# Kernel tuning notes

Hardware: AMD Instinct MI355X
Metric: run time of the kernel (lower is better)

The kernel has to match this reference:

```python
import jax, jax.numpy as jnp
import numpy as np

HIDDEN = 1024
NH = 16
NKV = 8
HD = 128
ROPE_BASE = 1e6
EPS = 1e-6


def _rms_norm(x, w):
    # x: [..., HD], norm in fp32 like the torch module
    xf = x.astype(jnp.float32)
    var = jnp.mean(xf * xf, axis=-1, keepdims=True)
    return w * (xf * jax.lax.rsqrt(var + EPS)).astype(x.dtype)


def _rotate_half(x):
    h = x.shape[-1] // 2
    return jnp.concatenate([-x[..., h:], x[..., :h]], axis=-1)


def _rope_cos_sin(position_ids, dtype):
    inv_freq = 1.0 / (ROPE_BASE ** (jnp.arange(0, HD, 2, dtype=jnp.float32) / HD))
    freqs = position_ids.astype(jnp.float32)[:, None] * inv_freq[None, :]  # [S, HD/2]
    emb = jnp.concatenate([freqs, freqs], axis=-1)  # [S, HD]
    return jnp.cos(emb).astype(dtype), jnp.sin(emb).astype(dtype)


def setup_inputs() -> dict:
    key = jax.random.key(0)
    ks = jax.random.split(key, 7)
    B, S = 2, 2048
    scale = lambda fan_in: 1.0 / np.sqrt(fan_in)
    return {
        "hidden_states": jax.random.normal(ks[0], (B, S, HIDDEN), jnp.float32),
        "position_ids": jnp.arange(S, dtype=jnp.int32),
        "Wq": jax.random.normal(ks[1], (HIDDEN, NH * HD), jnp.float32) * scale(HIDDEN),
        "Wk": jax.random.normal(ks[2], (HIDDEN, NKV * HD), jnp.float32) * scale(HIDDEN),
        "Wv": jax.random.normal(ks[3], (HIDDEN, NKV * HD), jnp.float32) * scale(HIDDEN),
        "Wo": jax.random.normal(ks[4], (NH * HD, HIDDEN), jnp.float32) * scale(NH * HD),
        "q_norm_w": jnp.ones((HD,), jnp.float32),
        "k_norm_w": jnp.ones((HD,), jnp.float32),
    }


def reference(hidden_states, position_ids, Wq, Wk, Wv, Wo, q_norm_w, k_norm_w):
    B, S, _ = hidden_states.shape
    G = NH // NKV  # GQA group size

    q = (hidden_states @ Wq).reshape(B, S, NH, HD)
    k = (hidden_states @ Wk).reshape(B, S, NKV, HD)
    v = (hidden_states @ Wv).reshape(B, S, NKV, HD)

    q = _rms_norm(q, q_norm_w).transpose(0, 2, 1, 3)  # [B, NH, S, HD]
    k = _rms_norm(k, k_norm_w).transpose(0, 2, 1, 3)  # [B, NKV, S, HD]
    v = v.transpose(0, 2, 1, 3)                        # [B, NKV, S, HD]

    cos, sin = _rope_cos_sin(position_ids, q.dtype)    # [S, HD] each
    q = q * cos + _rotate_half(q) * sin
    k = k * cos + _rotate_half(k) * sin

    # GQA: broadcast KV heads across groups instead of repeat_interleave copies
    qg = q.reshape(B, NKV, G, S, HD)
    scores = jnp.einsum('bkgsd,bknd->bkgsn', qg, k) / jnp.sqrt(jnp.float32(HD))
    causal = jnp.tril(jnp.ones((S, S), dtype=bool))
    scores = jnp.where(causal, scores, -jnp.inf)
    attn = jax.nn.softmax(scores, axis=-1)
    out = jnp.einsum('bkgsn,bknd->bkgsd', attn, v)  # [B, NKV, G, S, HD]
    out = out.reshape(B, NH, S, HD).transpose(0, 2, 1, 3).reshape(B, S, NH * HD)
    return out @ Wo
```

## Files before the change

### kernel.cpp

```cpp
#include <hip/hip_runtime.h>
#include <cstdint>
#include <cstddef>

#define HIDDEN 1024
#define NH 16
#define NKV 8
#define HD 128
#define SEQ 2048
#define BATCH 2
#define NTOK (BATCH*SEQ)

typedef __bf16 bf16x8 __attribute__((ext_vector_type(8)));
typedef float f32x4 __attribute__((ext_vector_type(4)));

__device__ __forceinline__ unsigned short f2bf(float f) {
  unsigned int u = __float_as_uint(f);
  u += 0x7FFFu + ((u >> 16) & 1u);
  return (unsigned short)(u >> 16);
}
__device__ __forceinline__ float bf2f(unsigned short h) {
  return __uint_as_float(((unsigned int)h) << 16);
}

#if __has_builtin(__builtin_amdgcn_exp2f)
#define EXP2(x) __builtin_amdgcn_exp2f(x)
#else
#define EXP2(x) exp2f(x)
#endif

__device__ __forceinline__ void glds16(const unsigned short* g, unsigned short* l) {
  __builtin_amdgcn_global_load_lds(
      (const __attribute__((address_space(1))) unsigned int*)g,
      (__attribute__((address_space(3))) unsigned int*)l, 16, 0, 0);
}

#define WAIT_VM8()   __builtin_amdgcn_s_waitcnt(0x0F78)
#define WAIT_VM4()   __builtin_amdgcn_s_waitcnt(0x0F74)
#define WAIT_VM0()   __builtin_amdgcn_s_waitcnt(0x0F70)
#define WAIT_LGKM0() __builtin_amdgcn_s_waitcnt(0xC07F)
#define BARRIER()    __builtin_amdgcn_s_barrier()

__device__ __forceinline__ float dpp_addx1(float x) {
  int v = __builtin_amdgcn_update_dpp(0, __float_as_int(x), 0xB1, 0xF, 0xF, true);
  return x + __int_as_float(v);
}

__global__ __launch_bounds__(256) void tcvt_all_kernel(
    const float* __restrict__ Wq, const float* __restrict__ Wk,
    const float* __restrict__ Wv, const float* __restrict__ Wo,
    const float* __restrict__ hs,
    unsigned short* __restrict__ wqkvt, unsigned short* __restrict__ wot,
    unsigned short* __restrict__ hsb) {
  const int i = blockIdx.x;
  const int tx = threadIdx.x, ty = threadIdx.y;
  if (i >= 6144) {
    const int t = ty*32 + tx;
    const size_t base = (size_t)(i - 6144) * 1024;
#pragma unroll
    for (int j = 0; j < 4; ++j) {
      const size_t idx = base + j*256 + t;
      float4 v = ((const float4*)hs)[idx];
      ushort4 o;
      o.x = f2bf(v.x); o.y = f2bf(v.y); o.z = f2bf(v.z); o.w = f2bf(v.w);
      ((ushort4*)hsb)[idx] = o;
    }
    return;
  }
  __shared__ float tl[32][33];
  const float* src; unsigned short* dst; int R, C, r0, c0;
  if (i < 2048)      { int l = i;        src = Wq; dst = wqkvt;                      R = 1024; C = 2048; r0 = (l & 31)*32; c0 = (l >> 5)*32; }
  else if (i < 3072) { int l = i - 2048; src = Wk; dst = wqkvt + (size_t)2048*1024;  R = 1024; C = 1024; r0 = (l & 31)*32; c0 = (l >> 5)*32; }
  else if (i < 4096) { int l = i - 3072; src = Wv; dst = wqkvt + (size_t)3072*1024;  R = 1024; C = 1024; r0 = (l & 31)*32; c0 = (l >> 5)*32; }
  else               { int l = i - 4096; src = Wo; dst = wot;                        R = 2048; C = 1024; r0 = (l & 63)*32; c0 = (l >> 6)*32; }
#pragma unroll
  for (int k = 0; k < 4; ++k)
    tl[ty + 8*k][tx] = src[(size_t)(r0 + ty + 8*k)*C + c0 + tx];
  __syncthreads();
#pragma unroll
  for (int k = 0; k < 4; ++k)
    dst[(size_t)(c0 + ty + 8*k)*R + r0 + tx] = f2bf(tl[tx][ty + 8*k]);
}

__global__ __launch_bounds__(256) void gemm_qkv_fused_kernel(
    const unsigned short* __restrict__ A,
    const unsigned short* __restrict__ Bt,
    const float* __restrict__ qw, const float* __restrict__ kw,
    const int* __restrict__ pos_ids,
    unsigned short* __restrict__ q_l,
    unsigned short* __restrict__ k_l,
    unsigned short* __restrict__ vt8) {
  constexpr int BM = 128, BK = 64, K = 1024, NIT = K/BK;
  constexpr int FS = 132;
  __shared__ __align__(16) char smem[70144];
  unsigned short* As0 = (unsigned short*)smem;
  unsigned short* Bs0 = (unsigned short*)(smem + 32768);
  float* ftile = (float*)smem;
  float* rinv  = (float*)(smem + 69632);

  const int t = threadIdx.x, lane = t & 63, w = t >> 6;
  const int l15 = lane & 15, l4 = lane >> 4;
  const int wr = (w >> 1)*64, wc = (w & 1)*64;
  const int m0 = blockIdx.x * BM, n0 = blockIdx.y * 128;
  const unsigned short* Ab = A + (size_t)m0*K;
  const unsigned short* Bb = Bt + (size_t)n0*K;

  const f32x4 vzero = {0.f, 0.f, 0.f, 0.f};
  f32x4 acc[4][4];
#pragma unroll
  for (int i = 0; i < 4; ++i)
#pragma unroll
    for (int j = 0; j < 4; ++j) acc[i][j] = vzero;

#pragma unroll
  for (int i = 0; i < 4; ++i) {
    const int c = (w*4 + i)*64 + lane;
    glds16(Ab + (size_t)(c >> 3)*K + ((c ^ (c >> 3)) & 7)*8, As0 + (size_t)(w*4 + i)*512);
  }
#pragma unroll
  for (int i = 0; i < 4; ++i) {
    const int c = (w*4 + i)*64 + lane;
    glds16(Bb + (size_t)(c >> 3)*K + ((c ^ (c >> 3)) & 7)*8, Bs0 + (size_t)(w*4 + i)*512);
  }

  for (int kb = 0; kb < NIT; ++kb) {
    const int cur = kb & 1;
    WAIT_LGKM0(); BARRIER();
    if (kb + 1 < NIT) {
      const int kn = (kb + 1) * BK;
      const int nb = (cur^1)*8192;
#pragma unroll
      for (int i = 0; i < 4; ++i) {
        const int c = (w*4 + i)*64 + lane;
        glds16(Ab + (size_t)(c >> 3)*K + kn + ((c ^ (c >> 3)) & 7)*8, As0 + nb + (size_t)(w*4 + i)*512);
      }
#pragma unroll
      for (int i = 0; i < 4; ++i) {
        const int c = (w*4 + i)*64 + lane;
        glds16(Bb + (size_t)(c >> 3)*K + kn + ((c ^ (c >> 3)) & 7)*8, Bs0 + nb + (size_t)(w*4 + i)*512);
      }
      WAIT_VM8();
    } else {
      WAIT_VM0();
    }
    BARRIER();

    const unsigned short* Ac = As0 + cur*8192;
    const unsigned short* Bc = Bs0 + cur*8192;
#pragma unroll
    for (int kk = 0; kk < 2; ++kk) {
      const int kc = kk*4 + l4;
      bf16x8 af[4], bfr[4];
#pragma unroll
      for (int i = 0; i < 4; ++i) {
        int m = wr + i*16 + l15;
        af[i] = *(const bf16x8*)(Ac + ((size_t)m*8 + (kc ^ (m & 7)))*8);
      }
#pragma unroll
      for (int j = 0; j < 4; ++j) {
        int n = wc + j*16 + l15;
        bfr[j] = *(const bf16x8*)(Bc + ((size_t)n*8 + (kc ^ (n & 7)))*8);
      }
#pragma unroll
      for (int i = 0; i < 4; ++i)
#pragma unroll
        for (int j = 0; j < 4; ++j)
          acc[i][j] = __builtin_amdgcn_mfma_f32_16x16x32_bf16(af[i], bfr[j], acc[i][j], 0, 0, 0);
    }
  }

  WAIT_LGKM0(); BARRIER();
#pragma unroll
  for (int i = 0; i < 4; ++i)
#pragma unroll
    for (int j = 0; j < 4; ++j)
#pragma unroll
      for (int r = 0; r < 4; ++r) {
        const int row = wr + i*16 + l4*4 + r;
        const int col = wc + j*16 + l15;
        ftile[row*FS + col] = acc[i][j][r];
      }
  WAIT_LGKM0(); BARRIER();

  const int ny = n0 >> 7;
  const int S0 = m0 & (SEQ-1);
  const int bb = m0 >> 11;

  if (ny < 24) {
    const bool isQ = ny < 16;
    {
      const int row = t >> 1, h2 = t & 1;
      const float* fr = ftile + row*FS + h2*64;
      float ssq = 0.f;
#pragma unroll
      for (int c = 0; c < 16; ++c) {
        float4 v = *(const float4*)(fr + 4*c);
        ssq += v.x*v.x + v.y*v.y + v.z*v.z + v.w*v.w;
      }
      ssq = dpp_addx1(ssq);
      if (h2 == 0) rinv[row] = rsqrtf(ssq*(1.0f/128.0f) + 1e-6f);
    }
    WAIT_LGKM0(); BARRIER();
    const float* wgt = isQ ? qw : kw;
    const int d = t & 127, rh = t >> 7;
    const float wd = wgt[d];
    const float w2 = wgt[d ^ 64];
    const float sgn = (d < 64) ? -1.f : 1.f;
    const float sOut = isQ ? 0.12751744f : 1.f;
    const float invf = exp2f(-(float)(d & 63) * 0.31143075889569023f);
    const int pos0 = pos_ids[S0 + rh*64];
    float cs, sn, dc, dsn;
    __sincosf((float)pos0 * invf, &sn, &cs);
    __sincosf(invf, &dsn, &dc);
    const int head = isQ ? ny : (ny - 16);
    unsigned short* dstb = isQ ? (q_l + ((size_t)(bb*NH + head)*SEQ + S0)*HD)
                               : (k_l + ((size_t)(bb*NKV + head)*SEQ + S0)*HD);
#pragma unroll 4
    for (int k = 0; k < 64; ++k) {
      const int row = rh*64 + k;
      const float r  = rinv[row];
      const float x1 = ftile[row*FS + d];
      const float x2 = ftile[row*FS + (d ^ 64)];
      const float y1 = x1*r*wd, y2 = x2*r*w2;
      const float o  = (y1*cs + sgn*(y2*sn)) * sOut;
      dstb[(size_t)row*HD + d] = f2bf(o);
      const float c2 = cs*dc - sn*dsn;
      sn = sn*dc + cs*dsn; cs = c2;
    }
  } else {
    const int vh = ny - 24;
    unsigned short* vb = vt8 + (size_t)(bb*NKV + vh)*HD*SEQ;
    const int d = t & 127, sbh = t >> 7;
#pragma unroll
    for (int sb = 0; sb < 8; ++sb) {
      const int sl = sbh*8 + sb;
      const int blk = sl >> 3, s = sl & 7;
      const int base_r = blk*64 + ((s>>2)<<5) + (((s>>1)&1)<<3) + ((s&1)<<2);
      union { unsigned short u[8]; uint4 q; } pk;
#pragma unroll
      for (int s8 = 0; s8 < 8; ++s8) {
        const int row = base_r + ((s8>>2)<<4) + (((s8>>1)&1)<<1) + (s8&1);
        pk.u[s8] = f2bf(ftile[row*FS + d]);
      }
      *(uint4*)(vb + ((size_t)((S0 >> 3) + sl)*128 + d)*8) = pk.q;
    }
  }
}

__global__ __launch_bounds__(256) void gemm_out_kernel(
    const unsigned short* __restrict__ A,
    const unsigned short* __restrict__ Bt,
    float* __restrict__ Cout, int M, int N, int K) {
  constexpr int BK = 64;
  __shared__ unsigned short As[2][128*BK];
  __shared__ unsigned short Bs[2][128*BK];
  const int t = threadIdx.x, lane = t & 63, w = t >> 6;
  const int l15 = lane & 15, l4 = lane >> 4;
  const int wr = (w >> 1)*64, wc = (w & 1)*64;
  const int m0 = blockIdx.y * 128, n0 = blockIdx.x * 128;
  const unsigned short* Ab = A + (size_t)m0*K;
  const unsigned short* Bb = Bt + (size_t)n0*K;

  const f32x4 vzero = {0.f, 0.f, 0.f, 0.f};
  f32x4 acc[4][4];
#pragma unroll
  for (int i = 0; i < 4; ++i)
#pragma unroll
    for (int j = 0; j < 4; ++j) acc[i][j] = vzero;

  const int NIT = K / BK;
#pragma unroll
  for (int i = 0; i < 4; ++i) {
    const int c = (w*4 + i)*64 + lane;
    glds16(Ab + (size_t)(c >> 3)*K + ((c ^ (c >> 3)) & 7)*8, &As[0][(size_t)(w*4 + i)*512]);
  }
#pragma unroll
  for (int i = 0; i < 4; ++i) {
    const int c = (w*4 + i)*64 + lane;
    glds16(Bb + (size_t)(c >> 3)*K + ((c ^ (c >> 3)) & 7)*8, &Bs[0][(size_t)(w*4 + i)*512]);
  }

  for (int kb = 0; kb < NIT; ++kb) {
    const int cur = kb & 1;
    WAIT_LGKM0(); BARRIER();
    if (kb + 1 < NIT) {
      const int kn = (kb + 1) * BK;
#pragma unroll
      for (int i = 0; i < 4; ++i) {
        const int c = (w*4 + i)*64 + lane;
        glds16(Ab + (size_t)(c >> 3)*K + kn + ((c ^ (c >> 3)) & 7)*8, &As[cur^1][(size_t)(w*4 + i)*512]);
      }
#pragma unroll
      for (int i = 0; i < 4; ++i) {
        const int c = (w*4 + i)*64 + lane;
        glds16(Bb + (size_t)(c >> 3)*K + kn + ((c ^ (c >> 3)) & 7)*8, &Bs[cur^1][(size_t)(w*4 + i)*512]);
      }
      WAIT_VM8();
    } else {
      WAIT_VM0();
    }
    BARRIER();

#pragma unroll
    for (int kk = 0; kk < 2; ++kk) {
      const int kc = kk*4 + l4;
      bf16x8 af[4], bfr[4];
#pragma unroll
      for (int i = 0; i < 4; ++i) {
        int m = wr + i*16 + l15;
        af[i] = *(const bf16x8*)(&As[cur][((size_t)m*8 + (kc ^ (m & 7)))*8]);
      }
#pragma unroll
      for (int j = 0; j < 4; ++j) {
        int n = wc + j*16 + l15;
        bfr[j] = *(const bf16x8*)(&Bs[cur][((size_t)n*8 + (kc ^ (n & 7)))*8]);
      }
#pragma unroll
      for (int i = 0; i < 4; ++i)
#pragma unroll
        for (int j = 0; j < 4; ++j)
          acc[i][j] = __builtin_amdgcn_mfma_f32_16x16x32_bf16(af[i], bfr[j], acc[i][j], 0, 0, 0);
    }
  }
#pragma unroll
  for (int i = 0; i < 4; ++i)
#pragma unroll
    for (int j = 0; j < 4; ++j)
#pragma unroll
      for (int r = 0; r < 4; ++r) {
        int row = m0 + wr + i*16 + l4*4 + r;
        int col = n0 + wc + j*16 + l15;
        Cout[(size_t)row*N + col] = acc[i][j][r];
      }
}

__global__ __launch_bounds__(256, 2) void attn_kernel(
    const unsigned short* __restrict__ q_l,
    const unsigned short* __restrict__ k_l,
    const unsigned short* __restrict__ vt8,
    unsigned short* __restrict__ o_part,
    float* __restrict__ l_part) {
  __shared__ __align__(16) char smem[65536];
  unsigned short* Ks0  = (unsigned short*)smem;
  unsigned short* Vts0 = (unsigned short*)(smem + 32768);

  const int t = threadIdx.x;
  const int lane = t & 63;
  const int w = t >> 6;
  const int l15 = lane & 15, l4 = lane >> 4;
  const int hb = blockIdx.x;
  const int h = hb & 15, b = hb >> 4;
  const int y = blockIdx.y;
  const int qt = 15 - (y >> 1);
  const int half = y & 1;
  const int kvh = h >> 1;
  const int q0 = qt * 128;
  const int kt0 = half ? (qt + 1) : 0;
  const int kt1 = half ? (2*qt + 2) : (qt + 1);

  const unsigned short* Kg = k_l + ((size_t)(b*NKV + kvh)*SEQ)*HD;
  const unsigned short* Vg = vt8 + (size_t)(b*NKV + kvh)*HD*SEQ;
  const unsigned short* Qbase = q_l + ((size_t)(b*NH + h)*SEQ)*HD;

  const f32x4 vzero = {0.f,0.f,0.f,0.f};
  union { unsigned int u[4]; bf16x8 v; } vones;
#pragma unroll
  for (int i = 0; i < 4; ++i) vones.u[i] = 0x3F803F80u;

  bf16x8 qf[2][4];
#pragma unroll
  for (int i = 0; i < 2; ++i) {
    const int row = q0 + w*32 + i*16 + l15;
    const unsigned short* Qp = Qbase + (size_t)row*HD;
#pragma unroll
    for (int kk = 0; kk < 4; ++kk)
      qf[i][kk] = *(const bf16x8*)(Qp + kk*32 + l4*8);
  }

  f32x4 oacc[2][8];
#pragma unroll
  for (int i = 0; i < 2; ++i)
#pragma unroll
    for (int jd = 0; jd < 8; ++jd) oacc[i][jd] = vzero;
  f32x4 oextra[2];
#pragma unroll
  for (int i = 0; i < 2; ++i) oextra[i] = vzero;

  {
    const int k00 = kt0 * 64;
#pragma unroll
    for (int i = 0; i < 4; ++i) {
      const int kc = w*4 + i;
      const int m = lane ^ (kc & 7);
      glds16(Kg + (size_t)(k00 + m)*HD + kc*8, Ks0 + (size_t)kc*64*8);
    }
#pragma unroll
    for (int i = 0; i < 4; ++i) {
      const int id = w*4 + i;
      const int skc = id >> 1, hh = id & 1;
      const int d = (hh*64 + lane) ^ skc;
      glds16(Vg + ((size_t)((k00 >> 3) + skc)*128 + d)*8, Vts0 + (size_t)(skc*128 + hh*64)*8);
    }
  }

#pragma unroll 1
  for (int kt = kt0; kt < kt1; ++kt) {
    const int cur = (kt - kt0) & 1;
    const int k0 = kt * 64;
    WAIT_LGKM0(); BARRIER();
    if (kt + 1 < kt1) {
      const int kn = k0 + 64;
      unsigned short* Ksn  = Ks0  + (cur^1)*8192;
      unsigned short* Vtsn = Vts0 + (cur^1)*8192;
#pragma unroll
      for (int i = 0; i < 4; ++i) {
        const int kc = w*4 + i;
        const int m = lane ^ (kc & 7);
        glds16(Kg + (size_t)(kn + m)*HD + kc*8, Ksn + (size_t)kc*64*8);
      }
#pragma unroll
      for (int i = 0; i < 4; ++i) {
        const int id = w*4 + i;
        const int skc = id >> 1, hh = id & 1;
        const int d = (hh*64 + lane) ^ skc;
        glds16(Vg + ((size_t)((kn >> 3) + skc)*128 + d)*8, Vtsn + (size_t)(skc*128 + hh*64)*8);
      }
      WAIT_VM8();
    } else {
      WAIT_VM0();
    }
    BARRIER();

    const unsigned short* KsC  = Ks0  + cur*8192;
    const unsigned short* VtsC = Vts0 + cur*8192;

    f32x4 sacc[4][2];
#pragma unroll
    for (int j = 0; j < 4; ++j)
#pragma unroll
      for (int i = 0; i < 2; ++i) sacc[j][i] = vzero;
    __builtin_amdgcn_s_setprio(1);
#pragma unroll
    for (int kk = 0; kk < 4; ++kk) {
      const int kc = kk*4 + l4;
      bf16x8 kb[4];
#pragma unroll
      for (int j = 0; j < 4; ++j) {
        int n = j*16 + l15;
        kb[j] = *(const bf16x8*)(KsC + ((size_t)kc*64 + (n ^ (kc & 7)))*8);
      }
#pragma unroll
      for (int j = 0; j < 4; ++j)
#pragma unroll
        for (int i = 0; i < 2; ++i)
          sacc[j][i] = __builtin_amdgcn_mfma_f32_16x16x32_bf16(kb[j], qf[i][kk], sacc[j][i], 0,0,0);
    }
    __builtin_amdgcn_s_setprio(0);

    const bool diag = (kt >= 2*qt);
#pragma unroll
    for (int j = 0; j < 2; ++j)
#pragma unroll
      for (int i = 0; i < 2; ++i)
#pragma unroll
        for (int r = 0; r < 4; ++r) {
          float sv = sacc[j][i][r];
          if (diag) {
            const int kvg = k0 + j*16 + l4*4 + r;
            const int qg  = q0 + w*32 + i*16 + l15;
            sv = (kvg > qg) ? -INFINITY : sv;
          }
          sacc[j][i][r] = EXP2(sv);
        }

    {
      union { unsigned int u[4]; bf16x8 v; } pb[2];
#pragma unroll
      for (int i = 0; i < 2; ++i) {
        const f32x4 t0 = sacc[0][i], t1 = sacc[1][i];
        pb[i].u[0] = (__float_as_uint(t0[0]) >> 16) | (__float_as_uint(t0[1]) & 0xFFFF0000u);
        pb[i].u[1] = (__float_as_uint(t0[2]) >> 16) | (__float_as_uint(t0[3]) & 0xFFFF0000u);
        pb[i].u[2] = (__float_as_uint(t1[0]) >> 16) | (__float_as_uint(t1[1]) & 0xFFFF0000u);
        pb[i].u[3] = (__float_as_uint(t1[2]) >> 16) | (__float_as_uint(t1[3]) & 0xFFFF0000u);
      }
      const int s = l4;
      __builtin_amdgcn_s_setprio(1);
#pragma unroll
      for (int td = 0; td < 8; ++td) {
        const int dd = td*16 + l15;
        bf16x8 va = *(const bf16x8*)(VtsC + ((size_t)s*128 + (dd ^ s))*8);
#pragma unroll
        for (int i = 0; i < 2; ++i)
          oacc[i][td] = __builtin_amdgcn_mfma_f32_16x16x32_bf16(va, pb[i].v, oacc[i][td], 0,0,0);
      }
#pragma unroll
      for (int i = 0; i < 2; ++i)
        oextra[i] = __builtin_amdgcn_mfma_f32_16x16x32_bf16(vones.v, pb[i].v, oextra[i], 0,0,0);
      __builtin_amdgcn_s_setprio(0);

#pragma unroll
      for (int j = 2; j < 4; ++j)
#pragma unroll
        for (int i = 0; i < 2; ++i)
#pragma unroll
          for (int r = 0; r < 4; ++r) {
            float sv = sacc[j][i][r];
            if (diag) {
              const int kvg = k0 + j*16 + l4*4 + r;
              const int qg  = q0 + w*32 + i*16 + l15;
              sv = (kvg > qg) ? -INFINITY : sv;
            }
            sacc[j][i][r] = EXP2(sv);
          }
    }

    {
      union { unsigned int u[4]; bf16x8 v; } pb[2];
#pragma unroll
      for (int i = 0; i < 2; ++i) {
        const f32x4 t0 = sacc[2][i], t1 = sacc[3][i];
        pb[i].u[0] = (__float_as_uint(t0[0]) >> 16) | (__float_as_uint(t0[1]) & 0xFFFF0000u);
        pb[i].u[1] = (__float_as_uint(t0[2]) >> 16) | (__float_as_uint(t0[3]) & 0xFFFF0000u);
        pb[i].u[2] = (__float_as_uint(t1[0]) >> 16) | (__float_as_uint(t1[1]) & 0xFFFF0000u);
        pb[i].u[3] = (__float_as_uint(t1[2]) >> 16) | (__float_as_uint(t1[3]) & 0xFFFF0000u);
      }
      const int s = 4 + l4;
      __builtin_amdgcn_s_setprio(1);
#pragma unroll
      for (int td = 0; td < 8; ++td) {
        const int dd = td*16 + l15;
        bf16x8 va = *(const bf16x8*)(VtsC + ((size_t)s*128 + (dd ^ s))*8);
#pragma unroll
        for (int i = 0; i < 2; ++i)
          oacc[i][td] = __builtin_amdgcn_mfma_f32_16x16x32_bf16(va, pb[i].v, oacc[i][td], 0,0,0);
      }
#pragma unroll
      for (int i = 0; i < 2; ++i)
        oextra[i] = __builtin_amdgcn_mfma_f32_16x16x32_bf16(vones.v, pb[i].v, oextra[i], 0,0,0);
      __builtin_amdgcn_s_setprio(0);
    }
  }

  unsigned short* ob = o_part + ((size_t)half*BATCH*NH*SEQ + (size_t)(b*NH + h)*SEQ)*HD;
  float* lb = l_part + (size_t)half*BATCH*NH*SEQ + (size_t)(b*NH + h)*SEQ;
#pragma unroll
  for (int i = 0; i < 2; ++i) {
    const float lsum = oextra[i][0];
    const float inv = (lsum > 0.f) ? 1.0f / lsum : 0.f;
    const int row = q0 + w*32 + i*16 + l15;
    if (l4 == 0) lb[row] = lsum;
#pragma unroll
    for (int td = 0; td < 8; ++td) {
      union { unsigned int u[2]; uint2 q; } pk;
      const float v0 = oacc[i][td][0]*inv, v1 = oacc[i][td][1]*inv;
      const float v2 = oacc[i][td][2]*inv, v3 = oacc[i][td][3]*inv;
      pk.u[0] = (unsigned int)f2bf(v0) | ((unsigned int)f2bf(v1) << 16);
      pk.u[1] = (unsigned int)f2bf(v2) | ((unsigned int)f2bf(v3) << 16);
      *(uint2*)(ob + (size_t)row*HD + td*16 + l4*4) = pk.q;
    }
  }
}

__global__ __launch_bounds__(256) void combine_kernel(
    const unsigned short* __restrict__ o_part,
    const float* __restrict__ l_part,
    unsigned short* __restrict__ attn_o) {
  const int tid = blockIdx.x * 256 + threadIdx.x;
  const int d8 = tid & 15;
  const int row = tid >> 4;
  const int s = row & (SEQ-1);
  const int bh = row >> 11;
  const int h = bh & 15, b = bh >> 4;
  const float la = l_part[row];
  const float lbv = l_part[BATCH*NH*SEQ + row];
  const float inv = 1.f / (la + lbv);
  const float wa = la * inv, wb = lbv * inv;
  const unsigned short* pa = o_part + (size_t)row*HD + d8*8;
  const unsigned short* pb = pa + (size_t)BATCH*NH*SEQ*HD;
  uint4 ua = *(const uint4*)pa;
  uint4 ub = *(const uint4*)pb;
  const unsigned short* ea = (const unsigned short*)&ua;
  const unsigned short* eb = (const unsigned short*)&ub;
  union { unsigned short u[8]; uint4 q; } o;
#pragma unroll
  for (int k = 0; k < 8; ++k)
    o.u[k] = f2bf(bf2f(ea[k])*wa + bf2f(eb[k])*wb);
  *(uint4*)(attn_o + ((size_t)(b*SEQ + s)*(NH*HD)) + h*HD + d8*8) = o.q;
}

extern "C" void kernel_launch(void* const* d_in, const int* in_sizes, int n_in,
                              void* d_out, int out_size, void* d_ws, size_t ws_size,
                              hipStream_t stream) {
  const float* hs = (const float*)d_in[0];
  const int* pos  = (const int*)d_in[1];
  const float* Wq = (const float*)d_in[2];
  const float* Wk = (const float*)d_in[3];
  const float* Wv = (const float*)d_in[4];
  const float* Wo = (const float*)d_in[5];
  const float* qw = (const float*)d_in[6];
  const float* kw = (const float*)d_in[7];
  float* out = (float*)d_out;
  char* ws = (char*)d_ws;

  unsigned short* attn_o = (unsigned short*)(ws + 0);
  unsigned short* wot    = (unsigned short*)(ws + ((size_t)16 << 20));
  unsigned short* q_l    = (unsigned short*)(ws + ((size_t)20 << 20));
  unsigned short* k_l    = (unsigned short*)(ws + ((size_t)36 << 20));
  unsigned short* vt8    = (unsigned short*)(ws + ((size_t)44 << 20));
  unsigned short* o_part = (unsigned short*)(ws + ((size_t)52 << 20));
  unsigned short* hsb    = (unsigned short*)(ws + ((size_t)52 << 20));
  unsigned short* wqkvt  = (unsigned short*)(ws + ((size_t)60 << 20));
  float*          l_part = (float*)(ws + ((size_t)84 << 20));

  tcvt_all_kernel<<<dim3(7168), dim3(32, 8), 0, stream>>>(Wq, Wk, Wv, Wo, hs, wqkvt, wot, hsb);
  gemm_qkv_fused_kernel<<<dim3(32, 32), dim3(256), 0, stream>>>(hsb, wqkvt, qw, kw, pos, q_l, k_l, vt8);
  attn_kernel<<<dim3(32, 32), dim3(256), 0, stream>>>(q_l, k_l, vt8, o_part, l_part);
  combine_kernel<<<dim3(4096), dim3(256), 0, stream>>>(o_part, l_part, attn_o);
  gemm_out_kernel<<<dim3(8, 32), dim3(256), 0, stream>>>(attn_o, wot, out, 4096, 1024, 2048);
}
```

Before: 236.7 us.

## Fuse split-KV combine into output projection GEMM A-tile loading

Removes the separate combine kernel and its attn_o round trip. The output GEMM now loads both partial attention outputs and their l sums directly through registers, merges and rounds them to bf16, and writes the result into the LDS A tile. The next tile's loads are issued before the MFMA loop and the merge runs after it, which overlaps the extra latency. In exchange, each of the 8 column blocks repeats the combine for its rows, reading o_part twice and doing the combine ALU work eight times, and the A path loses the direct global-to-LDS load.

```diff
diff --git a/kernel.cpp b/kernel.cpp
--- a/kernel.cpp
+++ b/kernel.cpp
@@ -34,8 +34,8 @@
       (__attribute__((address_space(3))) unsigned int*)l, 16, 0, 0);
 }
 
+#define WAIT_VM20()  __builtin_amdgcn_s_waitcnt(0x4F74)
 #define WAIT_VM8()   __builtin_amdgcn_s_waitcnt(0x0F78)
-#define WAIT_VM4()   __builtin_amdgcn_s_waitcnt(0x0F74)
 #define WAIT_VM0()   __builtin_amdgcn_s_waitcnt(0x0F70)
 #define WAIT_LGKM0() __builtin_amdgcn_s_waitcnt(0xC07F)
 #define BARRIER()    __builtin_amdgcn_s_barrier()
@@ -246,19 +246,31 @@
   }
 }
 
-__global__ __launch_bounds__(256) void gemm_out_kernel(
-    const unsigned short* __restrict__ A,
+__global__ __launch_bounds__(256) void gemm_out_fused_kernel(
+    const unsigned short* __restrict__ o_part,
+    const float* __restrict__ l_part,
     const unsigned short* __restrict__ Bt,
-    float* __restrict__ Cout, int M, int N, int K) {
-  constexpr int BK = 64;
+    float* __restrict__ Cout) {
+  constexpr int N = 1024, K = 2048, BK = 64, NIT = K/BK;
   __shared__ unsigned short As[2][128*BK];
   __shared__ unsigned short Bs[2][128*BK];
   const int t = threadIdx.x, lane = t & 63, w = t >> 6;
   const int l15 = lane & 15, l4 = lane >> 4;
   const int wr = (w >> 1)*64, wc = (w & 1)*64;
   const int m0 = blockIdx.y * 128, n0 = blockIdx.x * 128;
-  const unsigned short* Ab = A + (size_t)m0*K;
   const unsigned short* Bb = Bt + (size_t)n0*K;
+
+  int mS[4], kqS[4];
+  size_t rowS[4];
+#pragma unroll
+  for (int i = 0; i < 4; ++i) {
+    const int c = (w*4 + i)*64 + lane;
+    const int m = c >> 3;
+    mS[i] = m;
+    kqS[i] = (c ^ m) & 7;
+    const int token = m0 + m;
+    rowS[i] = (size_t)((token >> 11)*NH)*SEQ + (token & (SEQ-1));
+  }
 
   const f32x4 vzero = {0.f, 0.f, 0.f, 0.f};
   f32x4 acc[4][4];
@@ -267,34 +279,58 @@
 #pragma unroll
     for (int j = 0; j < 4; ++j) acc[i][j] = vzero;
 
-  const int NIT = K / BK;
-#pragma unroll
-  for (int i = 0; i < 4; ++i) {
-    const int c = (w*4 + i)*64 + lane;
-    glds16(Ab + (size_t)(c >> 3)*K + ((c ^ (c >> 3)) & 7)*8, &As[0][(size_t)(w*4 + i)*512]);
-  }
-#pragma unroll
-  for (int i = 0; i < 4; ++i) {
-    const int c = (w*4 + i)*64 + lane;
-    glds16(Bb + (size_t)(c >> 3)*K + ((c ^ (c >> 3)) & 7)*8, &Bs[0][(size_t)(w*4 + i)*512]);
+  {
+    const int h = 0, dbase = 0;
+#pragma unroll
+    for (int i = 0; i < 4; ++i) {
+      const size_t row = rowS[i] + (size_t)h*SEQ;
+      const unsigned short* pa = o_part + row*HD + dbase + kqS[i]*8;
+      const unsigned short* pbp = pa + (size_t)BATCH*NH*SEQ*HD;
+      uint4 ua = *(const uint4*)pa;
+      uint4 ub = *(const uint4*)pbp;
+      const float la = l_part[row];
+      const float lbv = l_part[(size_t)BATCH*NH*SEQ + row];
+      const float inv = 1.f/(la + lbv);
+      const float wa = la*inv, wb = lbv*inv;
+      const unsigned short* ea = (const unsigned short*)&ua;
+      const unsigned short* eb = (const unsigned short*)&ub;
+      union { unsigned short u[8]; uint4 q; } o;
+#pragma unroll
+      for (int e = 0; e < 8; ++e)
+        o.u[e] = f2bf(bf2f(ea[e])*wa + bf2f(eb[e])*wb);
+      *(uint4*)(&As[0][(size_t)(w*4 + i)*512 + lane*8]) = o.q;
+    }
+#pragma unroll
+    for (int i = 0; i < 4; ++i) {
+      const int c = (w*4 + i)*64 + lane;
+      glds16(Bb + (size_t)(c >> 3)*K + ((c ^ (c >> 3)) & 7)*8, &Bs[0][(size_t)(w*4 + i)*512]);
+    }
   }
 
   for (int kb = 0; kb < NIT; ++kb) {
     const int cur = kb & 1;
     WAIT_LGKM0(); BARRIER();
-    if (kb + 1 < NIT) {
+    const bool pk = (kb + 1 < NIT);
+    uint4 a0[4], a1[4];
+    float sla[4], slb[4];
+    if (pk) {
       const int kn = (kb + 1) * BK;
-#pragma unroll
-      for (int i = 0; i < 4; ++i) {
-        const int c = (w*4 + i)*64 + lane;
-        glds16(Ab + (size_t)(c >> 3)*K + kn + ((c ^ (c >> 3)) & 7)*8, &As[cur^1][(size_t)(w*4 + i)*512]);
+      const int h = kn >> 7, dbase = kn & 127;
+#pragma unroll
+      for (int i = 0; i < 4; ++i) {
+        const size_t row = rowS[i] + (size_t)h*SEQ;
+        const unsigned short* pa = o_part + row*HD + dbase + kqS[i]*8;
+        a0[i] = *(const uint4*)pa;
+        a1[i] = *(const uint4*)(pa + (size_t)BATCH*NH*SEQ*HD);
+        sla[i] = l_part[row];
+        slb[i] = l_part[(size_t)BATCH*NH*SEQ + row];
       }
 #pragma unroll
       for (int i = 0; i < 4; ++i) {
         const int c = (w*4 + i)*64 + lane;
         glds16(Bb + (size_t)(c >> 3)*K + kn + ((c ^ (c >> 3)) & 7)*8, &Bs[cur^1][(size_t)(w*4 + i)*512]);
       }
-      WAIT_VM8();
+      WAIT_VM20();
     } else {
       WAIT_VM0();
     }
@@ -320,7 +356,23 @@
         for (int j = 0; j < 4; ++j)
           acc[i][j] = __builtin_amdgcn_mfma_f32_16x16x32_bf16(af[i], bfr[j], acc[i][j], 0, 0, 0);
     }
-  }
+
+    if (pk) {
+#pragma unroll
+      for (int i = 0; i < 4; ++i) {
+        const float inv = 1.f/(sla[i] + slb[i]);
+        const float wa = sla[i]*inv, wb = slb[i]*inv;
+        const unsigned short* ea = (const unsigned short*)&a0[i];
+        const unsigned short* eb = (const unsigned short*)&a1[i];
+        union { unsigned short u[8]; uint4 q; } o;
+#pragma unroll
+        for (int e = 0; e < 8; ++e)
+          o.u[e] = f2bf(bf2f(ea[e])*wa + bf2f(eb[e])*wb);
+        *(uint4*)(&As[cur^1][(size_t)(w*4 + i)*512 + lane*8]) = o.q;
+      }
+    }
+  }
+
 #pragma unroll
   for (int i = 0; i < 4; ++i)
 #pragma unroll
@@ -560,33 +612,6 @@
   }
 }
 
-__global__ __launch_bounds__(256) void combine_kernel(
-    const unsigned short* __restrict__ o_part,
-    const float* __restrict__ l_part,
-    unsigned short* __restrict__ attn_o) {
-  const int tid = blockIdx.x * 256 + threadIdx.x;
-  const int d8 = tid & 15;
-  const int row = tid >> 4;
-  const int s = row & (SEQ-1);
-  const int bh = row >> 11;
-  const int h = bh & 15, b = bh >> 4;
-  const float la = l_part[row];
-  const float lbv = l_part[BATCH*NH*SEQ + row];
-  const float inv = 1.f / (la + lbv);
-  const float wa = la * inv, wb = lbv * inv;
-  const unsigned short* pa = o_part + (size_t)row*HD + d8*8;
-  const unsigned short* pb = pa + (size_t)BATCH*NH*SEQ*HD;
-  uint4 ua = *(const uint4*)pa;
-  uint4 ub = *(const uint4*)pb;
-  const unsigned short* ea = (const unsigned short*)&ua;
-  const unsigned short* eb = (const unsigned short*)&ub;
-  union { unsigned short u[8]; uint4 q; } o;
-#pragma unroll
-  for (int k = 0; k < 8; ++k)
-    o.u[k] = f2bf(bf2f(ea[k])*wa + bf2f(eb[k])*wb);
-  *(uint4*)(attn_o + ((size_t)(b*SEQ + s)*(NH*HD)) + h*HD + d8*8) = o.q;
-}
-
 extern "C" void kernel_launch(void* const* d_in, const int* in_sizes, int n_in,
                               void* d_out, int out_size, void* d_ws, size_t ws_size,
                               hipStream_t stream) {
@@ -601,7 +626,6 @@
   float* out = (float*)d_out;
   char* ws = (char*)d_ws;
 
-  unsigned short* attn_o = (unsigned short*)(ws + 0);
   unsigned short* wot    = (unsigned short*)(ws + ((size_t)16 << 20));
   unsigned short* q_l    = (unsigned short*)(ws + ((size_t)20 << 20));
   unsigned short* k_l    = (unsigned short*)(ws + ((size_t)36 << 20));
@@ -614,6 +638,5 @@
   tcvt_all_kernel<<<dim3(7168), dim3(32, 8), 0, stream>>>(Wq, Wk, Wv, Wo, hs, wqkvt, wot, hsb);
   gemm_qkv_fused_kernel<<<dim3(32, 32), dim3(256), 0, stream>>>(hsb, wqkvt, qw, kw, pos, q_l, k_l, vt8);
   attn_kernel<<<dim3(32, 32), dim3(256), 0, stream>>>(q_l, k_l, vt8, o_part, l_part);
-  combine_kernel<<<dim3(4096), dim3(256), 0, stream>>>(o_part, l_part, attn_o);
-  gemm_out_kernel<<<dim3(8, 32), dim3(256), 0, stream>>>(attn_o, wot, out, 4096, 1024, 2048);
-}
+  gemm_out_fused_kernel<<<dim3(8, 32), dim3(256), 0, stream>>>(o_part, l_part, wot, out);
+}
```

Result: slower. 258.7 us (+9.3%).
